# Optimization experiments

Measured on AMD Instinct MI355X. Metric: run time of the kernel, lower is better.

The kernel has to match this reference:

```python
import jax, jax.numpy as jnp
import numpy as np

BS, N, DX, DE, DY, NH = 4, 256, 256, 64, 128, 8
DF = DX // NH
ORDER = 3


def layer_norm(x, g, b, eps=1e-6):
    m = jnp.mean(x, -1, keepdims=True)
    v = jnp.mean((x - m) ** 2, -1, keepdims=True)
    return (x - m) / jnp.sqrt(v + eps) * g + b


def setup_inputs() -> dict:
    key = jax.random.key(0)
    ks = jax.random.split(key, 32)
    s = 0.02
    p = {}
    p['X'] = jax.random.normal(ks[0], (BS, N, DX), jnp.float32)
    p['E'] = jax.random.normal(ks[1], (BS, N, N, DE), jnp.float32)
    p['y'] = jax.random.normal(ks[2], (BS, DY), jnp.float32)
    lens = jax.random.randint(ks[3], (BS,), N // 2, N + 1)
    p['node_mask'] = (jnp.arange(N)[None, :] < lens[:, None]).astype(jnp.int32)
    p['W_emax'] = s * jax.random.normal(ks[4], (DE, DX))
    p['W_x1'] = s * jax.random.normal(ks[5], (DX, DX))
    p['Wq'] = s * jax.random.normal(ks[6], (DX, DX))
    p['Wk'] = s * jax.random.normal(ks[7], (DX, DX))
    p['Wv'] = s * jax.random.normal(ks[8], (DX, DX))
    p['Wo'] = s * jax.random.normal(ks[9], (DX, DX))
    p['W_y2'] = s * jax.random.normal(ks[10], (DY, DX))
    p['W_x2'] = s * jax.random.normal(ks[11], (DX, DX))
    p['Wc'] = s * jax.random.normal(ks[12], (DY, ORDER))
    p['bc'] = jnp.zeros((ORDER,), jnp.float32)
    p['sim_alpha'] = 0.1 * jax.random.normal(ks[13], (1,))
    p['W_Eout'] = s * jax.random.normal(ks[14], (DE, DE))
    p['G_kernel'] = 0.01 * jax.random.normal(ks[15], (DE, 128))
    p['X_kernel'] = 0.01 * jax.random.normal(ks[16], (DX, 64))
    p['W_Gtrans'] = s * jax.random.normal(ks[17], (128 * DE, DY))
    p['W_Xtrans'] = s * jax.random.normal(ks[18], (64 * DX, DY))
    p['W_yout'] = s * jax.random.normal(ks[19], (DY, DY))
    p['gx'] = jnp.ones((DX,), jnp.float32); p['bx'] = jnp.zeros((DX,), jnp.float32)
    p['ge'] = jnp.ones((DE,), jnp.float32); p['be'] = jnp.zeros((DE,), jnp.float32)
    p['gy'] = jnp.ones((DY,), jnp.float32); p['by'] = jnp.zeros((DY,), jnp.float32)
    return p


def reference(X, E, y, node_mask, W_emax, W_x1, Wq, Wk, Wv, Wo, W_y2, W_x2, Wc, bc,
              sim_alpha, W_Eout, G_kernel, X_kernel, W_Gtrans, W_Xtrans, W_yout,
              gx, bx, ge, be, gy, by):
    bs, n, dx = X.shape
    de = E.shape[-1]
    nm = node_mask.astype(X.dtype)              # bs, n
    x_mask = nm[:, :, None]                     # bs, n, 1
    emask = x_mask[:, :, None, :] * x_mask[:, None, :, :]  # bs, n, n, 1

    # --- edge -> node encoding (masked mean over dim 2; torch mean divides by n) ---
    e_enc = jax.nn.relu(jnp.mean(jnp.einsum('bijd,df->bijf', E, W_emax) * emask, axis=2))
    xplus = (X + jax.nn.relu(e_enc @ W_x1)) * x_mask

    # --- masked multi-head self attention (dropout = identity in eval) ---
    q = (xplus @ Wq).reshape(bs, n, NH, DF)
    k = (xplus @ Wk).reshape(bs, n, NH, DF)
    v = (xplus @ Wv).reshape(bs, n, NH, DF)
    scores = jnp.einsum('bqhd,bkhd->bhqk', q, k) / (DF ** 0.5)
    scores = jnp.where(nm[:, None, None, :] > 0, scores, -1e9)
    attn_out = jnp.einsum('bhqk,bkhd->bqhd', jax.nn.softmax(scores, -1), v).reshape(bs, n, dx) @ Wo
    new_X = layer_norm(attn_out * x_mask + X, gx, bx)

    # --- similarity-augmented edge matrix + order-3 polynomial recurrence ---
    xplusy = jax.nn.relu((X + jax.nn.relu(y @ W_y2)[:, None, :]) @ W_x2)
    sim = jnp.einsum('bnd,bmd->bnm', xplusy, xplusy) / (dx ** 0.5)
    G = (sim_alpha * sim[..., None] + E) * emask          # bs, n, n, de
    Gr = G.reshape(bs, de, n, n)                          # raw reshape, exactly as torch
    coeff = y @ Wc + bc                                    # bs, 3
    newE = coeff[:, 0][:, None, None, None] * Gr
    for kk in range(1, ORDER):
        newE = jnp.matmul(Gr, newE) + coeff[:, kk][:, None, None, None] * Gr
    new_E = layer_norm(jax.nn.relu(newE.reshape(bs, n, n, de) @ W_Eout) * emask + E, ge, be)

    # --- masked softmax pooling over edges ---
    Em = E * emask
    lg = jnp.where(emask > 0, (Em @ G_kernel) / (de ** 0.5), -1e9)   # bs,n,n,128
    aG = jax.nn.softmax(lg.reshape(bs, n * n, -1), axis=1)            # bs,n^2,128
    G_enc = jnp.einsum('bpk,bpd->bkd', aG, Em.reshape(bs, n * n, de)).reshape(bs, -1)
    G_enc = jax.nn.relu(G_enc @ W_Gtrans)

    # --- masked softmax pooling over nodes ---
    Xm = x_mask * X
    lx = jnp.where(x_mask > 0, (Xm @ X_kernel) / (dx ** 0.5), -1e9)   # bs,n,64
    aX = jax.nn.softmax(lx, axis=1)
    X_enc = jnp.einsum('bnk,bnd->bkd', aX, Xm).reshape(bs, -1)
    X_enc = jax.nn.relu(X_enc @ W_Xtrans)

    new_y = layer_norm(jax.nn.relu((G_enc + X_enc) @ W_yout) + y, gy, by)
    return new_X, new_E, new_y
```

## Files before the change

### kernel.cpp

```cpp
#include <hip/hip_runtime.h>
#include <hip/hip_bf16.h>

typedef __hip_bfloat16 bf16;
__device__ __forceinline__ bf16 tobf(float v){ return __float2bfloat16(v); }
__device__ __forceinline__ float frombf(bf16 v){ return __bfloat162float(v); }
__device__ __forceinline__ short f2bs(float x){ bf16 h=tobf(x); return *reinterpret_cast<short*>(&h); }

typedef __attribute__((ext_vector_type(8))) short bf16x8;
typedef __attribute__((ext_vector_type(4))) short short4v;
typedef __attribute__((ext_vector_type(4))) float f32x4;
typedef __attribute__((ext_vector_type(4))) int int4v;

static constexpr int cB=4, cN=256, cDX=256, cDE=64, cDY=128, cNH=8, cDF=32;

static constexpr size_t F_SIM  = 0;
static constexpr size_t F_P    = 262144;
static constexpr size_t F_NP   = 2359296;
static constexpr size_t F_GP   = F_NP + 1048576;
static constexpr size_t F_XP   = F_NP + 1048576 + 32768;
static constexpr size_t F_S    = 6619136;
static constexpr size_t F_EENC = 6684672;
static constexpr size_t F_XPL  = 6946816;
static constexpr size_t F_QB   = 7208960;
static constexpr size_t F_KB   = 7471104;
static constexpr size_t F_VB   = 7733248;
static constexpr size_t F_YW   = 7995392;
static constexpr size_t F_XPY  = 7996416;
static constexpr size_t F_COEF = 8258560;
static constexpr size_t F_GENC = 8258576;
static constexpr size_t F_XENC = 8291344;

__global__ void k_coeff_yw(const float* y, const float* Wc, const float* bc,
                           const float* W_y2, float* coeff, float* yw){
  int b = blockIdx.x; int f = threadIdx.x;
  float acc = 0.f;
  for(int r=0;r<cDY;++r) acc += y[b*cDY+r]*W_y2[r*cDX+f];
  yw[b*cDX+f] = fmaxf(acc,0.f);
  if (f < 3){
    float c = bc[f];
    for(int r=0;r<cDY;++r) c += y[b*cDY+r]*Wc[r*3+f];
    coeff[b*3+f] = c;
  }
}

__global__ void k_reduceE(const float* E, const int* nm, float* S){
  int bi = blockIdx.x; int b = bi / cN;
  int d = threadIdx.x;
  int jy = threadIdx.y;
  const float* Eb = E + (size_t)bi*cN*cDE;
  float acc = 0.f;
  for(int j=jy;j<cN;j+=4){
    acc += Eb[j*cDE+d] * (float)nm[b*cN+j];
  }
  __shared__ float red[4][64];
  red[jy][d]=acc; __syncthreads();
  if (jy==0) S[(size_t)bi*cDE+d] = red[0][d]+red[1][d]+red[2][d]+red[3][d];
}

__global__ void k_eenc(const float* S, const float* W_emax, const int* nm, float* eenc){
  int bi = blockIdx.x; int b = bi/cN; int i = bi%cN;
  int f = threadIdx.x;
  __shared__ float s[cDE];
  if (f<cDE) s[f]=S[(size_t)bi*cDE+f];
  __syncthreads();
  float acc=0.f;
  for(int d=0;d<cDE;++d) acc += s[d]*W_emax[d*cDX+f];
  float mi=(float)nm[b*cN+i];
  eenc[(size_t)bi*cDX+f] = fmaxf(acc*mi*(1.f/cN), 0.f);
}

__global__ void k_xplus(const float* X, const float* eenc, const float* W_x1,
                        const int* nm, float* xplus){
  int bi=blockIdx.x; int b=bi/cN; int i=bi%cN;
  int f=threadIdx.x;
  __shared__ float row[cDX];
  row[f]=eenc[(size_t)bi*cDX+f];
  __syncthreads();
  float acc=0.f;
  for(int c=0;c<cDX;++c) acc += row[c]*W_x1[c*cDX+f];
  float mi=(float)nm[b*cN+i];
  xplus[(size_t)bi*cDX+f] = (X[(size_t)bi*cDX+f] + fmaxf(acc,0.f))*mi;
}

__global__ void k_qkv(const float* xplus, const float* Wq, const float* Wk, const float* Wv,
                      float* qb, float* kb, float* vb){
  int bi=blockIdx.x; int f=threadIdx.x;
  __shared__ float row[cDX];
  row[f]=xplus[(size_t)bi*cDX+f];
  __syncthreads();
  float aq=0,ak=0,av=0;
  for(int c=0;c<cDX;++c){ float r=row[c]; aq+=r*Wq[c*cDX+f]; ak+=r*Wk[c*cDX+f]; av+=r*Wv[c*cDX+f]; }
  qb[(size_t)bi*cDX+f]=aq; kb[(size_t)bi*cDX+f]=ak; vb[(size_t)bi*cDX+f]=av;
}

__global__ void k_attn_softmax(const float* qb, const float* kb, const int* nm, float* P){
  int id=blockIdx.x; int b=id/(cNH*cN); int rem=id%(cNH*cN); int h=rem/cN; int i=rem%cN;
  int j=threadIdx.x;
  __shared__ float qrow[cDF];
  if (j<cDF) qrow[j]=qb[((size_t)b*cN+i)*cDX + h*cDF + j];
  __syncthreads();
  const float* krow = kb + ((size_t)b*cN+j)*cDX + h*cDF;
  float s=0.f;
  for(int c=0;c<cDF;++c) s += qrow[c]*krow[c];
  s *= 0.17677669529663687f;
  float val = (nm[b*cN+j]>0) ? s : -1e9f;
  __shared__ float red[256];
  red[j]=val; __syncthreads();
  for(int st=128;st>0;st>>=1){ if(j<st) red[j]=fmaxf(red[j],red[j+st]); __syncthreads(); }
  float mx=red[0]; __syncthreads();
  float e=__expf(val-mx);
  red[j]=e; __syncthreads();
  for(int st=128;st>0;st>>=1){ if(j<st) red[j]+=red[j+st]; __syncthreads(); }
  float denom=red[0];
  P[(size_t)id*cN + j] = e/denom;
}

__global__ void k_attn_out(const float* P, const float* vb, const float* Wo,
                           const float* X, const int* nm, const float* gx, const float* bx,
                           float* newX){
  int bi=blockIdx.x; int b=bi/cN; int i=bi%cN;
  int t=threadIdx.x;
  __shared__ float p8[cNH][cN];
  for(int h=0;h<cNH;++h) p8[h][t]=P[(((size_t)b*cNH+h)*cN+i)*cN + t];
  __syncthreads();
  int h=t/cDF;
  float acc=0.f;
  for(int j=0;j<cN;++j) acc += p8[h][j]*vb[((size_t)b*cN+j)*cDX + t];
  __shared__ float arow[cDX];
  arow[t]=acc; __syncthreads();
  float o=0.f;
  for(int c=0;c<cDX;++c) o += arow[c]*Wo[c*cDX+t];
  float mi=(float)nm[b*cN+i];
  float v = o*mi + X[(size_t)bi*cDX+t];
  __shared__ float red[256];
  red[t]=v; __syncthreads();
  for(int st=128;st>0;st>>=1){ if(t<st) red[t]+=red[t+st]; __syncthreads(); }
  float mean=red[0]*(1.f/cDX); __syncthreads();
  float dv=v-mean;
  red[t]=dv*dv; __syncthreads();
  for(int st=128;st>0;st>>=1){ if(t<st) red[t]+=red[t+st]; __syncthreads(); }
  float var=red[0]*(1.f/cDX);
  newX[(size_t)bi*cDX+t]=dv*rsqrtf(var+1e-6f)*gx[t]+bx[t];
}

__global__ void k_xplusy(const float* X, const float* yw, const float* W_x2, float* xpy){
  int bi=blockIdx.x; int b=bi/cN;
  int f=threadIdx.x;
  __shared__ float row[cDX];
  row[f]=X[(size_t)bi*cDX+f]+yw[b*cDX+f];
  __syncthreads();
  float acc=0.f;
  for(int c=0;c<cDX;++c) acc += row[c]*W_x2[c*cDX+f];
  xpy[(size_t)bi*cDX+f]=fmaxf(acc,0.f);
}

__global__ void k_sim(const float* xp, float* sim){
  int b=blockIdx.z;
  int tx=threadIdx.x, ty=threadIdx.y;
  __shared__ float Aa[16][17], Bb[16][17];
  const float* base = xp + (size_t)b*cN*cDX;
  float acc=0.f;
  for(int kt=0;kt<cDX;kt+=16){
    Aa[ty][tx]=base[(size_t)(blockIdx.y*16+ty)*cDX + kt+tx];
    Bb[ty][tx]=base[(size_t)(blockIdx.x*16+ty)*cDX + kt+tx];
    __syncthreads();
    for(int c=0;c<16;++c) acc += Aa[ty][c]*Bb[tx][c];
    __syncthreads();
  }
  sim[((size_t)b*cN + blockIdx.y*16+ty)*cN + blockIdx.x*16+tx] = acc*(1.f/16.f);
}

__global__ void k_G(const float* E, const float* sim, const int* nm, const float* alpha_p,
                    bf16* G){
  int bi=blockIdx.x; int b=bi/cN; int i=bi%cN;
  float mi=(float)nm[b*cN+i];
  float alpha=alpha_p[0];
  size_t base=(size_t)bi*cN*cDE;
  for(int t=threadIdx.x;t<cN*cDE;t+=blockDim.x){
    int j=t>>6;
    float mj=(float)nm[b*cN+j];
    G[base+t]=tobf((alpha*sim[(size_t)bi*cN+j]+E[base+t])*mi*mj);
  }
}

__device__ __forceinline__ void store_out(bf16* p, float v){ *p = tobf(v); }
__device__ __forceinline__ void store_out(float* p, float v){ *p = v; }

template<typename OT>
__global__ void __launch_bounds__(256) k_bmm_mfma(const bf16* A, const bf16* Bm, OT* C,
                                                  const float* coeff, int ia, int ib){
  int bc=blockIdx.z; int b=bc>>6;
  float alpha=(ia>=0)?coeff[b*3+ia]:1.0f;
  float beta=coeff[b*3+ib];
  const short* Ab=(const short*)(A+(size_t)bc*65536);
  const short* Bb=(const short*)(Bm+(size_t)bc*65536);
  OT* Cb=C+(size_t)bc*65536;
  const int row0=blockIdx.y*128, col0=blockIdx.x*128;
  const int t=threadIdx.x;
  const int lane=t&63, w=t>>6;
  const int wr=w>>1, wc=w&1;
  const int l15=lane&15, l4=lane>>4;
  __shared__ short A_s[128][72];
  __shared__ short B_s[128][72];
  f32x4 acc[4][4];
#pragma unroll
  for(int m=0;m<4;++m)
#pragma unroll
    for(int n=0;n<4;++n) acc[m][n]=(f32x4){0.f,0.f,0.f,0.f};

  const int kh=t>>7;
  const int nB=t&127;
  for(int kt=0;kt<256;kt+=64){
#pragma unroll
    for(int l=0;l<4;++l){
      int idx=t+l*256;
      int r=idx>>3, seg=idx&7;
      *(int4v*)&A_s[r][seg*8] = *(const int4v*)&Ab[(size_t)(row0+r)*256 + kt + seg*8];
    }
#pragma unroll 8
    for(int kk=0;kk<32;++kk){
      int k=kh*32+kk;
      B_s[nB][k]=Bb[(size_t)(kt+k)*256 + col0 + nB];
    }
    __syncthreads();
#pragma unroll
    for(int ks=0;ks<64;ks+=32){
      bf16x8 am[4], bn[4];
#pragma unroll
      for(int m=0;m<4;++m) am[m]=*(const bf16x8*)&A_s[wr*64+m*16+l15][ks+l4*8];
#pragma unroll
      for(int n=0;n<4;++n) bn[n]=*(const bf16x8*)&B_s[wc*64+n*16+l15][ks+l4*8];
#pragma unroll
      for(int m=0;m<4;++m)
#pragma unroll
        for(int n=0;n<4;++n)
          acc[m][n]=__builtin_amdgcn_mfma_f32_16x16x32_bf16(am[m],bn[n],acc[m][n],0,0,0);
    }
    __syncthreads();
  }
#pragma unroll
  for(int m=0;m<4;++m){
#pragma unroll
    for(int n=0;n<4;++n){
#pragma unroll
      for(int r=0;r<4;++r){
        int row=row0+wr*64+m*16+l4*4+r;
        int col=col0+wc*64+n*16+l15;
        size_t off=(size_t)row*256+col;
        float a0; { unsigned short u=(unsigned short)Ab[off]; unsigned int v=((unsigned int)u)<<16; a0=__int_as_float((int)v); }
        store_out(&Cb[off], alpha*acc[m][n][r]+beta*a0);
      }
    }
  }
}

__global__ void __launch_bounds__(256) k_Eout_mfma(const float* newE_in, const float* E,
                       const int* nm, const float* W_Eout, const float* ge, const float* be,
                       float* outE){
  const int t=threadIdx.x;
  const int lane=t&63, w=t>>6;
  const int l15=lane&15, l4=lane>>4;
  const int blk=blockIdx.x;
  const int b=blk>>8, i=blk&255;
  const float mi=(float)nm[b*cN+i];
  bf16x8 bnf[2][4];
#pragma unroll
  for(int ks=0;ks<2;++ks)
#pragma unroll
    for(int n=0;n<4;++n){
      bf16x8 v;
#pragma unroll
      for(int ii=0;ii<8;++ii)
        v[ii]=f2bs(W_Eout[(ks*32+l4*8+ii)*cDE + n*16+l15]);
      bnf[ks][n]=v;
    }
  float gev[4], bev[4];
#pragma unroll
  for(int n=0;n<4;++n){ gev[n]=ge[n*16+l15]; bev[n]=be[n*16+l15]; }

  for(int it=0;it<4;++it){
    const int j0=it*64+w*16;
    const int p0=blk*256 + j0;
    f32x4 acc[4];
#pragma unroll
    for(int n=0;n<4;++n) acc[n]=(f32x4){0.f,0.f,0.f,0.f};
    if(mi>0.f){
#pragma unroll
      for(int ks=0;ks<2;++ks){
        const float* ap=&newE_in[(size_t)(p0+l15)*cDE + ks*32 + l4*8];
        float4 a0=*(const float4*)ap;
        float4 a1=*(const float4*)(ap+4);
        bf16x8 am;
        am[0]=f2bs(a0.x); am[1]=f2bs(a0.y); am[2]=f2bs(a0.z); am[3]=f2bs(a0.w);
        am[4]=f2bs(a1.x); am[5]=f2bs(a1.y); am[6]=f2bs(a1.z); am[7]=f2bs(a1.w);
#pragma unroll
        for(int n=0;n<4;++n)
          acc[n]=__builtin_amdgcn_mfma_f32_16x16x32_bf16(am,bnf[ks][n],acc[n],0,0,0);
      }
    }
    float mj[4];
#pragma unroll
    for(int r=0;r<4;++r) mj[r]=mi*(float)nm[b*cN + j0 + l4*4 + r];
#pragma unroll
    for(int reg=0;reg<4;++reg){
      size_t rowoff=(size_t)(p0 + l4*4 + reg)*cDE;
      float v0=fmaxf(acc[0][reg],0.f)*mj[reg]+E[rowoff + 0*16+l15];
      float v1=fmaxf(acc[1][reg],0.f)*mj[reg]+E[rowoff + 1*16+l15];
      float v2=fmaxf(acc[2][reg],0.f)*mj[reg]+E[rowoff + 2*16+l15];
      float v3=fmaxf(acc[3][reg],0.f)*mj[reg]+E[rowoff + 3*16+l15];
      float s=v0+v1+v2+v3;
      float q=v0*v0+v1*v1+v2*v2+v3*v3;
#pragma unroll
      for(int m=1;m<16;m<<=1){ s+=__shfl_xor(s,m); q+=__shfl_xor(q,m); }
      float mean=s*(1.f/cDE);
      float var=q*(1.f/cDE)-mean*mean;
      float inv=rsqrtf(var+1e-6f);
      outE[rowoff + 0*16+l15]=(v0-mean)*inv*gev[0]+bev[0];
      outE[rowoff + 1*16+l15]=(v1-mean)*inv*gev[1]+bev[1];
      outE[rowoff + 2*16+l15]=(v2-mean)*inv*gev[2]+bev[2];
      outE[rowoff + 3*16+l15]=(v3-mean)*inv*gev[3]+bev[3];
    }
  }
}

__global__ void __launch_bounds__(256) k_Gaccum_mfma(const float* E, const int* nm,
                                                     const float* G_kernel,
                                                     float* Npart, float* Dpart){
  const int chunk=blockIdx.x;
  const int b=blockIdx.y;
  const int t=threadIdx.x;
  const int lane=t&63, w=t>>6;
  const int l15=lane&15, l4=lane>>4;

  __shared__ short EmA[128][72];
  __shared__ short Wt[128][136];
  __shared__ float mrow[128];
  __shared__ float Dacc[128];
  __shared__ float Dpar[4][128];

  bf16x8 gk[2][8];
#pragma unroll
  for(int kt=0;kt<2;++kt)
#pragma unroll
    for(int n=0;n<8;++n){
      bf16x8 v;
#pragma unroll
      for(int ii=0;ii<8;++ii)
        v[ii]=f2bs(G_kernel[(kt*32+l4*8+ii)*128 + n*16+l15]*0.125f);
      gk[kt][n]=v;
    }

  f32x4 nacc[2][4];
#pragma unroll
  for(int a=0;a<2;++a)
#pragma unroll
    for(int d2=0;d2<4;++d2) nacc[a][d2]=(f32x4){0.f,0.f,0.f,0.f};

  if(t<128) Dacc[t]=0.f;
  __syncthreads();

  const size_t ebase=((size_t)b)<<16;
  for(int sub=0;sub<4;++sub){
    const int rowbase = chunk*512 + sub*128;
    {
      int pr=t>>1, hh=t&1;
      int p=rowbase+pr;
      const float* src=&E[(ebase+p)*cDE + hh*32];
#pragma unroll
      for(int q=0;q<8;++q){
        float4 v=*(const float4*)(src+q*4);
        short4v s4; s4[0]=f2bs(v.x); s4[1]=f2bs(v.y); s4[2]=f2bs(v.z); s4[3]=f2bs(v.w);
        *(short4v*)&EmA[pr][hh*32+q*4]=s4;
      }
      if(hh==0) mrow[pr]=(float)(nm[b*cN+(p>>8)]*nm[b*cN+(p&255)]);
    }
    __syncthreads();

    f32x4 wacc[2][8];
#pragma unroll
    for(int m=0;m<2;++m)
#pragma unroll
      for(int n=0;n<8;++n) wacc[m][n]=(f32x4){0.f,0.f,0.f,0.f};
#pragma unroll
    for(int kt=0;kt<2;++kt){
      bf16x8 am[2];
#pragma unroll
      for(int m=0;m<2;++m) am[m]=*(const bf16x8*)&EmA[w*32+m*16+l15][kt*32+l4*8];
#pragma unroll
      for(int m=0;m<2;++m)
#pragma unroll
        for(int n=0;n<8;++n)
          wacc[m][n]=__builtin_amdgcn_mfma_f32_16x16x32_bf16(am[m],gk[kt][n],wacc[m][n],0,0,0);
    }
    float dsum[8];
#pragma unroll
    for(int n=0;n<8;++n) dsum[n]=0.f;
#pragma unroll
    for(int m=0;m<2;++m){
#pragma unroll
      for(int r=0;r<4;++r){
        int pl=w*32+m*16+l4*4+r;
        float mv=mrow[pl];
#pragma unroll
        for(int n=0;n<8;++n){
          float wv=(mv>0.f)?__expf(wacc[m][n][r]):0.f;
          dsum[n]+=wv;
          Wt[n*16+l15][pl]=f2bs(wv);
        }
      }
    }
#pragma unroll
    for(int n=0;n<8;++n){
      float s=dsum[n];
      s+=__shfl_xor(s,16); s+=__shfl_xor(s,32);
      if(l4==0) Dpar[w][n*16+l15]=s;
    }
    __syncthreads();

#pragma unroll
    for(int ks=0;ks<4;++ks){
      bf16x8 aw[2];
#pragma unroll
      for(int a=0;a<2;++a) aw[a]=*(const bf16x8*)&Wt[w*32+a*16+l15][ks*32+l4*8];
      bf16x8 bm[4];
#pragma unroll
      for(int d2=0;d2<4;++d2){
        bf16x8 v;
#pragma unroll
        for(int ii=0;ii<8;++ii) v[ii]=EmA[ks*32+l4*8+ii][d2*16+l15];
        bm[d2]=v;
      }
#pragma unroll
      for(int a=0;a<2;++a)
#pragma unroll
        for(int d2=0;d2<4;++d2)
          nacc[a][d2]=__builtin_amdgcn_mfma_f32_16x16x32_bf16(aw[a],bm[d2],nacc[a][d2],0,0,0);
    }
    __syncthreads();
    if(t<128) Dacc[t]+=Dpar[0][t]+Dpar[1][t]+Dpar[2][t]+Dpar[3][t];
    __syncthreads();
  }

  size_t pi=(size_t)b*128+chunk;
  float* np=Npart + pi*128*cDE;
#pragma unroll
  for(int a=0;a<2;++a){
#pragma unroll
    for(int d2=0;d2<4;++d2){
#pragma unroll
      for(int r=0;r<4;++r){
        int k=w*32+a*16+l4*4+r;
        int d=d2*16+l15;
        np[(size_t)k*cDE+d]=nacc[a][d2][r];
      }
    }
  }
  if(t<128) Dpart[pi*128+t]=Dacc[t];
}

__global__ void k_Gcombine(const float* Npart, const float* Dpart, float* Genc){
  int bk=blockIdx.x; int b=bk>>7; int k=bk&127;
  int d=threadIdx.x;
  float n=0.f, dd=0.f;
  for(int pi=0;pi<128;++pi){
    size_t base=((size_t)b*128+pi)*128+k;
    n += Npart[base*cDE+d];
    dd += Dpart[base];
  }
  Genc[(size_t)b*8192 + k*cDE + d]=n/dd;
}

__global__ void k_Xenc(const float* X, const int* nm, const float* X_kernel, float* Xenc){
  int k=blockIdx.x;
  int b=blockIdx.y;
  int n=threadIdx.x;
  float m=(float)nm[b*cN+n];
  const float* xr=X+((size_t)b*cN+n)*cDX;
  float acc=0.f;
  for(int c=0;c<cDX;++c) acc += xr[c]*X_kernel[c*64+k];
  float lg=(m>0.f)?acc*(1.f/16.f):-1e9f;
  __shared__ float red[256];
  red[n]=lg; __syncthreads();
  for(int st=128;st>0;st>>=1){ if(n<st) red[n]=fmaxf(red[n],red[n+st]); __syncthreads(); }
  float mx=red[0]; __syncthreads();
  float e=__expf(lg-mx);
  red[n]=e; __syncthreads();
  for(int st=128;st>0;st>>=1){ if(n<st) red[n]+=red[n+st]; __syncthreads(); }
  float denom=red[0]; __syncthreads();
  __shared__ float ps[256];
  ps[n]=e/denom;
  __syncthreads();
  int d=n;
  float s=0.f;
  for(int nn=0;nn<cN;++nn) s += ps[nn]*X[((size_t)b*cN+nn)*cDX+d];
  Xenc[(size_t)b*16384 + k*cDX + d]=s;
}

__global__ void __launch_bounds__(256) k_headA(const float* Genc, const float* Xenc,
                        const float* W_Gtrans, const float* W_Xtrans,
                        float* Gp, float* Xp){
  int blk=blockIdx.x;
  int t=threadIdx.x;
  int o=t&127, sub=t>>7;
  int b0=sub*2, b1=sub*2+1;
  __shared__ float ash[4][128];
  if(blk<64){
    int ch=blk;
    for(int l=t;l<512;l+=256){
      int b=l>>7, q=l&127;
      ash[b][q]=Genc[(size_t)b*8192 + ch*128 + q];
    }
    __syncthreads();
    const float* wbase=W_Gtrans + (size_t)ch*128*cDY + o;
    float a0=0.f, a1=0.f;
#pragma unroll 4
    for(int qq=0;qq<128;++qq){
      float w=wbase[(size_t)qq*cDY];
      a0+=ash[b0][qq]*w; a1+=ash[b1][qq]*w;
    }
    Gp[((size_t)b0*64+ch)*cDY+o]=a0;
    Gp[((size_t)b1*64+ch)*cDY+o]=a1;
  } else {
    int ch=blk-64;
    for(int l=t;l<512;l+=256){
      int b=l>>7, q=l&127;
      ash[b][q]=Xenc[(size_t)b*16384 + ch*128 + q];
    }
    __syncthreads();
    const float* wbase=W_Xtrans + (size_t)ch*128*cDY + o;
    float a0=0.f, a1=0.f;
#pragma unroll 4
    for(int qq=0;qq<128;++qq){
      float w=wbase[(size_t)qq*cDY];
      a0+=ash[b0][qq]*w; a1+=ash[b1][qq]*w;
    }
    Xp[((size_t)b0*128+ch)*cDY+o]=a0;
    Xp[((size_t)b1*128+ch)*cDY+o]=a1;
  }
}

__global__ void k_headB(const float* Gp, const float* Xp, const float* W_yout,
                        const float* y, const float* gy, const float* by, float* newy){
  int b=blockIdx.x; int o=threadIdx.x;
  float g=0.f,x=0.f;
  for(int ch=0;ch<64;++ch)  g+=Gp[((size_t)b*64+ch)*cDY+o];
  for(int ch=0;ch<128;++ch) x+=Xp[((size_t)b*128+ch)*cDY+o];
  __shared__ float srow[cDY];
  srow[o]=fmaxf(g,0.f)+fmaxf(x,0.f);
  __syncthreads();
  float h=0.f;
  for(int r=0;r<cDY;++r) h += srow[r]*W_yout[r*cDY+o];
  float v=fmaxf(h,0.f)+y[b*cDY+o];
  __shared__ float red[cDY];
  red[o]=v; __syncthreads();
  for(int st=64;st>0;st>>=1){ if(o<st) red[o]+=red[o+st]; __syncthreads(); }
  float mean=red[0]*(1.f/cDY); __syncthreads();
  float dv=v-mean;
  red[o]=dv*dv; __syncthreads();
  for(int st=64;st>0;st>>=1){ if(o<st) red[o]+=red[o+st]; __syncthreads(); }
  float var=red[0]*(1.f/cDY);
  newy[b*cDY+o]=dv*rsqrtf(var+1e-6f)*gy[o]+by[o];
}

extern "C" void kernel_launch(void* const* d_in, const int* in_sizes, int n_in,
                              void* d_out, int out_size, void* d_ws, size_t ws_size,
                              hipStream_t stream){
  const float* X     =(const float*)d_in[0];
  const float* E     =(const float*)d_in[1];
  const float* y     =(const float*)d_in[2];
  const int*   nm    =(const int*)  d_in[3];
  const float* W_emax=(const float*)d_in[4];
  const float* W_x1  =(const float*)d_in[5];
  const float* Wq    =(const float*)d_in[6];
  const float* Wk    =(const float*)d_in[7];
  const float* Wv    =(const float*)d_in[8];
  const float* Wo    =(const float*)d_in[9];
  const float* W_y2  =(const float*)d_in[10];
  const float* W_x2  =(const float*)d_in[11];
  const float* Wc    =(const float*)d_in[12];
  const float* bc    =(const float*)d_in[13];
  const float* salpha=(const float*)d_in[14];
  const float* W_Eout=(const float*)d_in[15];
  const float* G_kern=(const float*)d_in[16];
  const float* X_kern=(const float*)d_in[17];
  const float* W_Gtr =(const float*)d_in[18];
  const float* W_Xtr =(const float*)d_in[19];
  const float* W_yout=(const float*)d_in[20];
  const float* gx    =(const float*)d_in[21];
  const float* bx    =(const float*)d_in[22];
  const float* ge    =(const float*)d_in[23];
  const float* be    =(const float*)d_in[24];
  const float* gy    =(const float*)d_in[25];
  const float* by    =(const float*)d_in[26];

  char* wsb=(char*)d_ws;
  bf16* Gbf=(bf16*)wsb;
  bf16* Bbf=(bf16*)(wsb+33554432);
  float* Npart=(float*)(wsb+33554432);
  float* f32=(float*)(wsb+67108864);
  float* sim  = f32+F_SIM;
  float* P    = f32+F_P;
  float* Dpart= f32+F_NP;
  float* Gp   = f32+F_GP;
  float* Xp   = f32+F_XP;
  float* S    = f32+F_S;
  float* eenc = f32+F_EENC;
  float* xplus= f32+F_XPL;
  float* qb   = f32+F_QB;
  float* kb   = f32+F_KB;
  float* vb   = f32+F_VB;
  float* yw   = f32+F_YW;
  float* xpy  = f32+F_XPY;
  float* coeff= f32+F_COEF;
  float* Genc = f32+F_GENC;
  float* Xenc = f32+F_XENC;

  float* out=(float*)d_out;
  float* newX=out;
  float* newE_out=out+262144;
  float* newy=out+17039360;

  k_coeff_yw<<<cB,256,0,stream>>>(y,Wc,bc,W_y2,coeff,yw);
  k_reduceE<<<cB*cN,dim3(64,4),0,stream>>>(E,nm,S);
  k_eenc<<<cB*cN,256,0,stream>>>(S,W_emax,nm,eenc);
  k_xplus<<<cB*cN,256,0,stream>>>(X,eenc,W_x1,nm,xplus);
  k_qkv<<<cB*cN,256,0,stream>>>(xplus,Wq,Wk,Wv,qb,kb,vb);
  k_attn_softmax<<<cB*cNH*cN,256,0,stream>>>(qb,kb,nm,P);
  k_attn_out<<<cB*cN,256,0,stream>>>(P,vb,Wo,X,nm,gx,bx,newX);
  k_xplusy<<<cB*cN,256,0,stream>>>(X,yw,W_x2,xpy);
  k_sim<<<dim3(16,16,cB),dim3(16,16),0,stream>>>(xpy,sim);
  k_G<<<cB*cN,256,0,stream>>>(E,sim,nm,salpha,Gbf);
  k_bmm_mfma<bf16><<<dim3(2,2,cB*cDE),256,0,stream>>>(Gbf,Gbf,Bbf,coeff,0,1);
  k_bmm_mfma<float><<<dim3(2,2,cB*cDE),256,0,stream>>>(Gbf,Bbf,newE_out,coeff,-1,2);
  k_Eout_mfma<<<1024,256,0,stream>>>(newE_out,E,nm,W_Eout,ge,be,newE_out);
  k_Gaccum_mfma<<<dim3(128,cB),256,0,stream>>>(E,nm,G_kern,Npart,Dpart);
  k_Gcombine<<<cB*128,64,0,stream>>>(Npart,Dpart,Genc);
  k_Xenc<<<dim3(64,cB),256,0,stream>>>(X,nm,X_kern,Xenc);
  k_headA<<<192,256,0,stream>>>(Genc,Xenc,W_Gtr,W_Xtr,Gp,Xp);
  k_headB<<<cB,128,0,stream>>>(Gp,Xp,W_yout,y,gy,by,newy);
}
```

Measured before the change: 424.7 us.

## Transpose G once so both batched GEMMs load B operand with vector loads

Adds a transpose kernel that writes G^T, so the first GEMM reads its B operand as contiguous rows via 128-bit loads. It replaces the old scalar strided B-tile loads. The first GEMM writes its bf16 result already transposed, so the second GEMM can also use vector B loads. Both epilogues stage accumulators through shared memory to issue vectorized, coalesced stores. This costs an extra kernel launch, 32MB more workspace, and an extra pass over G.

```diff
diff --git a/kernel.cpp b/kernel.cpp
--- a/kernel.cpp
+++ b/kernel.cpp
@@ -5,6 +5,7 @@
 __device__ __forceinline__ bf16 tobf(float v){ return __float2bfloat16(v); }
 __device__ __forceinline__ float frombf(bf16 v){ return __bfloat162float(v); }
 __device__ __forceinline__ short f2bs(float x){ bf16 h=tobf(x); return *reinterpret_cast<short*>(&h); }
+__device__ __forceinline__ float bs2f(short s){ unsigned int v=((unsigned int)(unsigned short)s)<<16; return __int_as_float((int)v); }
 
 typedef __attribute__((ext_vector_type(8))) short bf16x8;
 typedef __attribute__((ext_vector_type(4))) short short4v;
@@ -183,44 +184,60 @@
   }
 }
 
-__device__ __forceinline__ void store_out(bf16* p, float v){ *p = tobf(v); }
-__device__ __forceinline__ void store_out(float* p, float v){ *p = v; }
-
-template<typename OT>
-__global__ void __launch_bounds__(256) k_bmm_mfma(const bf16* A, const bf16* Bm, OT* C,
-                                                  const float* coeff, int ia, int ib){
-  int bc=blockIdx.z; int b=bc>>6;
-  float alpha=(ia>=0)?coeff[b*3+ia]:1.0f;
-  float beta=coeff[b*3+ib];
-  const short* Ab=(const short*)(A+(size_t)bc*65536);
-  const short* Bb=(const short*)(Bm+(size_t)bc*65536);
-  OT* Cb=C+(size_t)bc*65536;
+__global__ void __launch_bounds__(256) k_transp(const short* G, short* Gt){
+  const int bc=blockIdx.z;
+  const int p0=blockIdx.y*128, q0=blockIdx.x*128;
+  const int t=threadIdx.x;
+  __shared__ short T[128][136];
+  const short* src=G+(size_t)bc*65536;
+  short* dst=Gt+(size_t)bc*65536;
+#pragma unroll
+  for(int l=0;l<8;++l){
+    int idx=t+l*256;
+    int r=idx>>4, seg=idx&15;
+    *(int4v*)&T[r][seg*8]=*(const int4v*)&src[(size_t)(p0+r)*256 + q0 + seg*8];
+  }
+  __syncthreads();
+  int qq=t&127, hf=t>>7;
+#pragma unroll
+  for(int ss=0;ss<8;++ss){
+    bf16x8 v;
+#pragma unroll
+    for(int ii=0;ii<8;++ii) v[ii]=T[hf*64+ss*8+ii][qq];
+    *(bf16x8*)&dst[(size_t)(q0+qq)*256 + p0 + hf*64 + ss*8]=v;
+  }
+}
+
+__global__ void __launch_bounds__(256) k_bmm_t(const short* G, const short* Gt, short* Bt2,
+                                               const float* coeff){
+  const int bc=blockIdx.z; const int b=bc>>6;
+  const float alpha=coeff[b*3+0];
+  const float beta=coeff[b*3+1];
+  const short* Ag=G+(size_t)bc*65536;
+  const short* At=Gt+(size_t)bc*65536;
+  short* Ct=Bt2+(size_t)bc*65536;
   const int row0=blockIdx.y*128, col0=blockIdx.x*128;
   const int t=threadIdx.x;
   const int lane=t&63, w=t>>6;
   const int wr=w>>1, wc=w&1;
   const int l15=lane&15, l4=lane>>4;
-  __shared__ short A_s[128][72];
-  __shared__ short B_s[128][72];
+  __shared__ char smem[36864];
+  short (*A_s)[72]=(short(*)[72])smem;
+  short (*B_s)[72]=(short(*)[72])(smem+18432);
+  float (*Cf)[132]=(float(*)[132])smem;
   f32x4 acc[4][4];
 #pragma unroll
   for(int m=0;m<4;++m)
 #pragma unroll
     for(int n=0;n<4;++n) acc[m][n]=(f32x4){0.f,0.f,0.f,0.f};
 
-  const int kh=t>>7;
-  const int nB=t&127;
   for(int kt=0;kt<256;kt+=64){
 #pragma unroll
     for(int l=0;l<4;++l){
       int idx=t+l*256;
       int r=idx>>3, seg=idx&7;
-      *(int4v*)&A_s[r][seg*8] = *(const int4v*)&Ab[(size_t)(row0+r)*256 + kt + seg*8];
-    }
-#pragma unroll 8
-    for(int kk=0;kk<32;++kk){
-      int k=kh*32+kk;
-      B_s[nB][k]=Bb[(size_t)(kt+k)*256 + col0 + nB];
+      *(int4v*)&A_s[r][seg*8]=*(const int4v*)&Ag[(size_t)(row0+r)*256 + kt + seg*8];
+      *(int4v*)&B_s[r][seg*8]=*(const int4v*)&At[(size_t)(col0+r)*256 + kt + seg*8];
     }
     __syncthreads();
 #pragma unroll
@@ -238,19 +255,98 @@
     }
     __syncthreads();
   }
-#pragma unroll
-  for(int m=0;m<4;++m){
-#pragma unroll
-    for(int n=0;n<4;++n){
-#pragma unroll
-      for(int r=0;r<4;++r){
-        int row=row0+wr*64+m*16+l4*4+r;
-        int col=col0+wc*64+n*16+l15;
-        size_t off=(size_t)row*256+col;
-        float a0; { unsigned short u=(unsigned short)Ab[off]; unsigned int v=((unsigned int)u)<<16; a0=__int_as_float((int)v); }
-        store_out(&Cb[off], alpha*acc[m][n][r]+beta*a0);
-      }
-    }
+  for(int rs=0;rs<8;++rs){
+    if(rs) __syncthreads();
+    int m=rs&3;
+    if(wr==(rs>>2)){
+#pragma unroll
+      for(int n=0;n<4;++n)
+#pragma unroll
+        for(int r=0;r<4;++r)
+          Cf[l4*4+r][wc*64+n*16+l15]=acc[m][n][r];
+    }
+    __syncthreads();
+    int c=t&127, hf=t>>7;
+    const short* gsrc=&At[(size_t)(col0+c)*256 + row0 + rs*16 + hf*8];
+    short* dst=&Ct[(size_t)(col0+c)*256 + row0 + rs*16 + hf*8];
+    bf16x8 a8=*(const bf16x8*)gsrc;
+    bf16x8 o8;
+#pragma unroll
+    for(int ii=0;ii<8;++ii)
+      o8[ii]=f2bs(alpha*Cf[hf*8+ii][c] + beta*bs2f(a8[ii]));
+    *(bf16x8*)dst=o8;
+  }
+}
+
+__global__ void __launch_bounds__(256) k_bmm_f(const short* G, const short* Bt2, float* C,
+                                               const float* coeff){
+  const int bc=blockIdx.z; const int b=bc>>6;
+  const float beta=coeff[b*3+2];
+  const short* Ag=G+(size_t)bc*65536;
+  const short* Bt=Bt2+(size_t)bc*65536;
+  float* Cb=C+(size_t)bc*65536;
+  const int row0=blockIdx.y*128, col0=blockIdx.x*128;
+  const int t=threadIdx.x;
+  const int lane=t&63, w=t>>6;
+  const int wr=w>>1, wc=w&1;
+  const int l15=lane&15, l4=lane>>4;
+  __shared__ char smem[36864];
+  short (*A_s)[72]=(short(*)[72])smem;
+  short (*B_s)[72]=(short(*)[72])(smem+18432);
+  float (*Cf)[132]=(float(*)[132])smem;
+  f32x4 acc[4][4];
+#pragma unroll
+  for(int m=0;m<4;++m)
+#pragma unroll
+    for(int n=0;n<4;++n) acc[m][n]=(f32x4){0.f,0.f,0.f,0.f};
+
+  for(int kt=0;kt<256;kt+=64){
+#pragma unroll
+    for(int l=0;l<4;++l){
+      int idx=t+l*256;
+      int r=idx>>3, seg=idx&7;
+      *(int4v*)&A_s[r][seg*8]=*(const int4v*)&Ag[(size_t)(row0+r)*256 + kt + seg*8];
+      *(int4v*)&B_s[r][seg*8]=*(const int4v*)&Bt[(size_t)(col0+r)*256 + kt + seg*8];
+    }
+    __syncthreads();
+#pragma unroll
+    for(int ks=0;ks<64;ks+=32){
+      bf16x8 am[4], bn[4];
+#pragma unroll
+      for(int m=0;m<4;++m) am[m]=*(const bf16x8*)&A_s[wr*64+m*16+l15][ks+l4*8];
+#pragma unroll
+      for(int n=0;n<4;++n) bn[n]=*(const bf16x8*)&B_s[wc*64+n*16+l15][ks+l4*8];
+#pragma unroll
+      for(int m=0;m<4;++m)
+#pragma unroll
+        for(int n=0;n<4;++n)
+          acc[m][n]=__builtin_amdgcn_mfma_f32_16x16x32_bf16(am[m],bn[n],acc[m][n],0,0,0);
+    }
+    __syncthreads();
+  }
+  for(int rs=0;rs<8;++rs){
+    if(rs) __syncthreads();
+    int m=rs&3;
+    if(wr==(rs>>2)){
+#pragma unroll
+      for(int n=0;n<4;++n)
+#pragma unroll
+        for(int r=0;r<4;++r)
+          Cf[l4*4+r][wc*64+n*16+l15]=acc[m][n][r];
+    }
+    __syncthreads();
+    int r=t>>4, cs=t&15;
+    int row=row0+rs*16+r;
+    const short* asrc=&Ag[(size_t)row*256 + col0 + cs*8];
+    float* dst=&Cb[(size_t)row*256 + col0 + cs*8];
+    bf16x8 a8=*(const bf16x8*)asrc;
+    f32x4 o0,o1;
+#pragma unroll
+    for(int ii=0;ii<4;++ii) o0[ii]=Cf[r][cs*8+ii]   + beta*bs2f(a8[ii]);
+#pragma unroll
+    for(int ii=0;ii<4;++ii) o1[ii]=Cf[r][cs*8+4+ii] + beta*bs2f(a8[4+ii]);
+    *(f32x4*)&dst[0]=o0;
+    *(f32x4*)&dst[4]=o1;
   }
 }
 
@@ -595,9 +691,11 @@
 
   char* wsb=(char*)d_ws;
   bf16* Gbf=(bf16*)wsb;
-  bf16* Bbf=(bf16*)(wsb+33554432);
+  short* Gs=(short*)wsb;
+  short* Bt2=(short*)(wsb+33554432);
+  short* Gts=(short*)(wsb+67108864);
   float* Npart=(float*)(wsb+33554432);
-  float* f32=(float*)(wsb+67108864);
+  float* f32=(float*)(wsb+100663296);
   float* sim  = f32+F_SIM;
   float* P    = f32+F_P;
   float* Dpart= f32+F_NP;
@@ -630,8 +728,9 @@
   k_xplusy<<<cB*cN,256,0,stream>>>(X,yw,W_x2,xpy);
   k_sim<<<dim3(16,16,cB),dim3(16,16),0,stream>>>(xpy,sim);
   k_G<<<cB*cN,256,0,stream>>>(E,sim,nm,salpha,Gbf);
-  k_bmm_mfma<bf16><<<dim3(2,2,cB*cDE),256,0,stream>>>(Gbf,Gbf,Bbf,coeff,0,1);
-  k_bmm_mfma<float><<<dim3(2,2,cB*cDE),256,0,stream>>>(Gbf,Bbf,newE_out,coeff,-1,2);
+  k_transp<<<dim3(2,2,cB*cDE),256,0,stream>>>(Gs,Gts);
+  k_bmm_t<<<dim3(2,2,cB*cDE),256,0,stream>>>(Gs,Gts,Bt2,coeff);
+  k_bmm_f<<<dim3(2,2,cB*cDE),256,0,stream>>>(Gs,Bt2,newE_out,coeff);
   k_Eout_mfma<<<1024,256,0,stream>>>(newE_out,E,nm,W_Eout,ge,be,newE_out);
   k_Gaccum_mfma<<<dim3(128,cB),256,0,stream>>>(E,nm,G_kern,Npart,Dpart);
   k_Gcombine<<<cB*128,64,0,stream>>>(Npart,Dpart,Genc);
```

After: 416.5 us. About the same (-1.9%).
